# Performance work log

Hardware: AMD Instinct MI355X
Metric: run time of the kernel (lower is better)

Reference implementation:

```python
import jax, jax.numpy as jnp
import numpy as np

N = 16384
E = 524288
IN_DIM, H1, H2 = 256, 128, 64


def setup_inputs() -> dict:
    key = jax.random.key(0)
    ks = jax.random.split(key, 9)
    features = jax.random.normal(ks[0], (N, IN_DIM), dtype=jnp.float32)
    src = jax.random.randint(ks[1], (E,), 0, N, dtype=jnp.int32)
    dst = jax.random.randint(ks[2], (E,), 0, N, dtype=jnp.int32)
    s = 0.1
    W1 = jax.random.normal(ks[3], (IN_DIM, H1), dtype=jnp.float32) * s
    b1 = jnp.zeros((H1,), dtype=jnp.float32)
    W2 = jax.random.normal(ks[4], (H1, H1), dtype=jnp.float32) * s
    b2 = jnp.zeros((H1,), dtype=jnp.float32)
    W3 = jax.random.normal(ks[5], (H1, H2), dtype=jnp.float32) * s
    b3 = jnp.zeros((H2,), dtype=jnp.float32)
    return {"features": features, "src": src, "dst": dst,
            "W1": W1, "b1": b1, "W2": W2, "b2": b2, "W3": W3, "b3": b3}


def _degree_norms(src, dst):
    ones = jnp.ones(src.shape[0], dtype=jnp.float32)
    deg_out = jax.ops.segment_sum(ones, src, num_segments=N)
    deg_in = jax.ops.segment_sum(ones, dst, num_segments=N)
    # allow_zero_in_degree=True with norm='both': clamp degree to min 1
    norm_out = jax.lax.rsqrt(jnp.maximum(deg_out, 1.0))  # [N]
    norm_in = jax.lax.rsqrt(jnp.maximum(deg_in, 1.0))    # [N]
    return norm_out, norm_in


def _graph_conv(h, src, dst, norm_out, norm_in, W, b, relu):
    # DGL GraphConv, norm='both': D_in^{-1/2} A^T (D_out^{-1/2} h) W + b
    h = h * norm_out[:, None]
    msg = h[src]                                   # gather [E, d]
    agg = jax.ops.segment_sum(msg, dst, num_segments=N)  # scatter-add [N, d]
    out = agg * norm_in[:, None] @ W + b
    return jax.nn.relu(out) if relu else out


def reference(features, src, dst, W1, b1, W2, b2, W3, b3):
    norm_out, norm_in = _degree_norms(src, dst)
    h = _graph_conv(features, src, dst, norm_out, norm_in, W1, b1, True)
    h = _graph_conv(h, src, dst, norm_out, norm_in, W2, b2, True)
    z = _graph_conv(h, src, dst, norm_out, norm_in, W3, b3, False)  # [N, H2]
    adj_rec = jax.nn.sigmoid(z @ z.T)  # [N, N]
    return adj_rec, z
```

## Files before the change

### kernel.cpp

```cpp
#include <hip/hip_runtime.h>
#include <hip/hip_bf16.h>

#define NN 16384
#define EE 524288

constexpr int D0 = 256, D1 = 128, D2 = 64;

typedef __attribute__((ext_vector_type(8))) short short8;
typedef __attribute__((ext_vector_type(4))) float f32x4;

__device__ __forceinline__ float b2f(ushort u) {
  union { unsigned int i; float f; } x;
  x.i = ((unsigned int)u) << 16;
  return x.f;
}
__device__ __forceinline__ ushort f2b(float f) {
  __hip_bfloat16 h = __float2bfloat16(f);
  return *reinterpret_cast<ushort*>(&h);
}


__global__ __launch_bounds__(256) void count_deg_kernel(
    const int* __restrict__ src, const int* __restrict__ dst,
    int* __restrict__ deg_out, int* __restrict__ deg_in) {
  int e = blockIdx.x * 256 + threadIdx.x;
  if (e < EE) {
    atomicAdd(&deg_out[src[e]], 1);
    atomicAdd(&deg_in[dst[e]], 1);
  }
}

__global__ __launch_bounds__(256) void scan1_kernel(
    const int* __restrict__ deg_in, int* __restrict__ intra,
    int* __restrict__ part) {
  __shared__ int sc[256];
  int t = threadIdx.x;
  int v = blockIdx.x * 256 + t;
  int d = deg_in[v];
  sc[t] = d;
  __syncthreads();
  for (int off = 1; off < 256; off <<= 1) {
    int add = (t >= off) ? sc[t - off] : 0;
    __syncthreads();
    sc[t] += add;
    __syncthreads();
  }
  intra[v] = sc[t] - d;
  if (t == 255) part[blockIdx.x] = sc[255];
}

__global__ __launch_bounds__(64) void scan2_kernel(
    const int* __restrict__ part, int* __restrict__ partx) {
  __shared__ int p[64];
  int t = threadIdx.x;
  int d = part[t];
  p[t] = d;
  __syncthreads();
  for (int off = 1; off < 64; off <<= 1) {
    int add = (t >= off) ? p[t - off] : 0;
    __syncthreads();
    p[t] += add;
    __syncthreads();
  }
  partx[t] = p[t] - d;
}

__global__ __launch_bounds__(256) void scan3_kernel(
    const int* __restrict__ deg_in, const int* __restrict__ deg_out,
    const int* __restrict__ intra, const int* __restrict__ partx,
    int* __restrict__ row_ptr, int* __restrict__ cursor,
    float* __restrict__ norm_out, float* __restrict__ norm_in) {
  int t = threadIdx.x;
  int v = blockIdx.x * 256 + t;
  int rp = partx[blockIdx.x] + intra[v];
  row_ptr[v] = rp;
  cursor[v] = rp;
  norm_out[v] = rsqrtf(fmaxf((float)deg_out[v], 1.0f));
  norm_in[v]  = rsqrtf(fmaxf((float)deg_in[v], 1.0f));
  if (v == NN - 1) row_ptr[NN] = rp + deg_in[v];
}

__global__ __launch_bounds__(256) void fill_csr_kernel(
    const int* __restrict__ src, const int* __restrict__ dst,
    int* __restrict__ cursor, int* __restrict__ csr_src) {
  int e = blockIdx.x * 256 + threadIdx.x;
  if (e < EE) {
    int pos = atomicAdd(&cursor[dst[e]], 1);
    csr_src[pos] = src[e];
  }
}


template<int DIN, int DOUT, int KC, bool OBF16>
__global__ __launch_bounds__(256) void gemm_kernel(
    const float* __restrict__ h, const float* __restrict__ W,
    const float* __restrict__ norm_out, float* __restrict__ tf,
    ushort* __restrict__ tb) {
  constexpr int W4 = DOUT / 4;
  constexpr int RG = 256 / W4;
  constexpr int RPT = 32 / RG;
  __shared__ float A[32][DIN];
  __shared__ float WC[KC][DOUT];
  int tid = threadIdx.x;
  int r0 = blockIdx.x * 32;
  constexpr int NF4 = 32 * DIN / 4;
  for (int q = tid; q < NF4; q += 256) {
    int r = q / (DIN / 4);
    int c = q % (DIN / 4);
    float4 x = *(const float4*)&h[(size_t)(r0 + r) * DIN + c * 4];
    float no = norm_out[r0 + r];
    x.x *= no; x.y *= no; x.z *= no; x.w *= no;
    *(float4*)&A[r][c * 4] = x;
  }
  int c4 = tid % W4;
  int rg = tid / W4;
  float4 acc[RPT];
#pragma unroll
  for (int j = 0; j < RPT; ++j) acc[j] = make_float4(0.f, 0.f, 0.f, 0.f);

  for (int kc = 0; kc < DIN / KC; ++kc) {
    __syncthreads();
#pragma unroll
    for (int q = 0; q < KC * W4 / 256; ++q)
      ((float4*)WC)[q * 256 + tid] =
          ((const float4*)W)[(size_t)kc * KC * W4 + q * 256 + tid];
    __syncthreads();
#pragma unroll 4
    for (int k2 = 0; k2 < KC; ++k2) {
      float4 w = *(const float4*)&WC[k2][c4 * 4];
#pragma unroll
      for (int j = 0; j < RPT; ++j) {
        float a = A[rg + j * RG][kc * KC + k2];
        acc[j].x += a * w.x; acc[j].y += a * w.y;
        acc[j].z += a * w.z; acc[j].w += a * w.w;
      }
    }
  }
#pragma unroll
  for (int j = 0; j < RPT; ++j) {
    size_t row = (size_t)(r0 + rg + j * RG);
    if (OBF16) {
      ushort4 o;
      o.x = f2b(acc[j].x); o.y = f2b(acc[j].y);
      o.z = f2b(acc[j].z); o.w = f2b(acc[j].w);
      *(ushort4*)&tb[row * DOUT + c4 * 4] = o;
    } else {
      *(float4*)&tf[row * DOUT + c4 * 4] = acc[j];
    }
  }
}


template<int DOUT, bool RELU>
__global__ __launch_bounds__(256) void gather_bf16_kernel(
    const ushort* __restrict__ t, const float* __restrict__ bias,
    const float* __restrict__ norm_in, const int* __restrict__ row_ptr,
    const int* __restrict__ csr, float* __restrict__ out) {
  constexpr int G8 = DOUT / 8;
  constexpr int S = 256 / G8;
  __shared__ float red[S][G8][8];
  int tid = threadIdx.x;
  int c8 = tid % G8, slot = tid / G8;
  int v = blockIdx.x;
  int k0 = row_ptr[v], k1 = row_ptr[v + 1];
  float a[8];
#pragma unroll
  for (int i = 0; i < 8; ++i) a[i] = 0.f;
  for (int k = k0 + slot; k < k1; k += S) {
    int s = csr[k];
    short8 m = *(const short8*)&t[(size_t)s * DOUT + c8 * 8];
#pragma unroll
    for (int i = 0; i < 8; ++i) a[i] += b2f((ushort)m[i]);
  }
#pragma unroll
  for (int i = 0; i < 8; ++i) red[slot][c8][i] = a[i];
  __syncthreads();
#pragma unroll
  for (int s = S / 2; s >= 1; s >>= 1) {
    if (slot < s) {
#pragma unroll
      for (int i = 0; i < 8; ++i) red[slot][c8][i] += red[slot + s][c8][i];
    }
    __syncthreads();
  }
  if (tid < G8) {
    float ni = norm_in[v];
    float o[8];
#pragma unroll
    for (int i = 0; i < 8; ++i) {
      o[i] = red[0][tid][i] * ni + bias[tid * 8 + i];
      if (RELU) o[i] = fmaxf(o[i], 0.f);
    }
    *(float4*)&out[(size_t)v * DOUT + tid * 8] = make_float4(o[0], o[1], o[2], o[3]);
    *(float4*)&out[(size_t)v * DOUT + tid * 8 + 4] = make_float4(o[4], o[5], o[6], o[7]);
  }
}


template<int DOUT, bool RELU>
__global__ __launch_bounds__(256) void gather_f32_kernel(
    const float* __restrict__ t, const float* __restrict__ bias,
    const float* __restrict__ norm_in, const int* __restrict__ row_ptr,
    const int* __restrict__ csr, float* __restrict__ out,
    ushort* __restrict__ zb) {
  constexpr int W4 = DOUT / 4;
  constexpr int S = 256 / W4;
  __shared__ float4 red[256];
  int tid = threadIdx.x;
  int c4 = tid % W4, slot = tid / W4;
  int v = blockIdx.x;
  int k0 = row_ptr[v], k1 = row_ptr[v + 1];
  float4 acc = make_float4(0.f, 0.f, 0.f, 0.f);
  for (int k = k0 + slot; k < k1; k += S) {
    int s = csr[k];
    float4 m = *(const float4*)&t[(size_t)s * DOUT + c4 * 4];
    acc.x += m.x; acc.y += m.y; acc.z += m.z; acc.w += m.w;
  }
  red[tid] = acc;
  __syncthreads();
  if (tid < W4) {
    float4 a = red[tid];
#pragma unroll
    for (int s = 1; s < S; ++s) {
      float4 b = red[s * W4 + tid];
      a.x += b.x; a.y += b.y; a.z += b.z; a.w += b.w;
    }
    float ni = norm_in[v];
    float4 b4 = *(const float4*)&bias[tid * 4];
    a.x = a.x * ni + b4.x; a.y = a.y * ni + b4.y;
    a.z = a.z * ni + b4.z; a.w = a.w * ni + b4.w;
    if (RELU) {
      a.x = fmaxf(a.x, 0.f); a.y = fmaxf(a.y, 0.f);
      a.z = fmaxf(a.z, 0.f); a.w = fmaxf(a.w, 0.f);
    }
    *(float4*)&out[(size_t)v * DOUT + tid * 4] = a;
    ushort4 ob;
    ob.x = f2b(a.x); ob.y = f2b(a.y); ob.z = f2b(a.z); ob.w = f2b(a.w);
    *(ushort4*)&zb[(size_t)v * DOUT + tid * 4] = ob;
  }
}


__global__ __launch_bounds__(256) void adj_mfma_kernel(
    const ushort* __restrict__ zb, float* __restrict__ C) {
  __shared__ ushort SMEM[2 * 128 * 64];
  ushort* ZR = SMEM;
  ushort* ZC = SMEM + 128 * 64;
  int t = threadIdx.x;
  int bx = blockIdx.x & 127, by = blockIdx.x >> 7;
  int row0 = by * 128, col0 = bx * 128;
  {
    int r = t >> 1;
    int ub = (t & 1) * 4;
    const float4* zr = (const float4*)(zb + (size_t)(row0 + r) * 64);
    const float4* zc = (const float4*)(zb + (size_t)(col0 + r) * 64);
    float4* LR = (float4*)ZR;
    float4* LC = (float4*)ZC;
#pragma unroll
    for (int u = 0; u < 4; ++u) {
      int sw = (ub + u) ^ (r & 7);
      LR[r * 8 + sw] = zr[ub + u];
      LC[r * 8 + sw] = zc[ub + u];
    }
  }
  __syncthreads();
  int l = t & 63, w = t >> 6;
  int wy = w >> 1, wx = w & 1;
  int lr = l & 15, lg = l >> 4;
  f32x4 acc[4][4];
#pragma unroll
  for (int i = 0; i < 4; ++i)
#pragma unroll
    for (int j = 0; j < 4; ++j) acc[i][j] = (f32x4){0.f, 0.f, 0.f, 0.f};

#pragma unroll
  for (int ks = 0; ks < 2; ++ks) {
    short8 af[4], bf_[4];
    int u = ks * 4 + lg;
#pragma unroll
    for (int i = 0; i < 4; ++i) {
      int ar = wy * 64 + i * 16 + lr;
      af[i] = *(const short8*)&ZR[ar * 64 + ((u ^ (ar & 7)) << 3)];
      int ac = wx * 64 + i * 16 + lr;
      bf_[i] = *(const short8*)&ZC[ac * 64 + ((u ^ (ac & 7)) << 3)];
    }
#pragma unroll
    for (int i = 0; i < 4; ++i)
#pragma unroll
      for (int j = 0; j < 4; ++j)
        acc[i][j] = __builtin_amdgcn_mfma_f32_16x16x32_bf16(
            bf_[j], af[i], acc[i][j], 0, 0, 0);
  }

  __syncthreads();
  float* scr = ((float*)SMEM) + w * (16 * 68);
  int sr = l >> 4;
  int sc = (l & 15) * 4;
  float* Cbase = C + (size_t)(row0 + wy * 64) * NN + col0 + wx * 64 + sc;
#pragma unroll
  for (int i = 0; i < 4; ++i) {
#pragma unroll
    for (int j = 0; j < 4; ++j) {
      f32x4 o;
      o[0] = __builtin_amdgcn_rcpf(1.0f + __expf(-acc[i][j][0]));
      o[1] = __builtin_amdgcn_rcpf(1.0f + __expf(-acc[i][j][1]));
      o[2] = __builtin_amdgcn_rcpf(1.0f + __expf(-acc[i][j][2]));
      o[3] = __builtin_amdgcn_rcpf(1.0f + __expf(-acc[i][j][3]));
      *(f32x4*)&scr[lr * 68 + j * 16 + lg * 4] = o;
    }
    __syncthreads();
#pragma unroll
    for (int rp = 0; rp < 4; ++rp) {
      int rloc = rp * 4 + sr;
      float4 v = *(const float4*)&scr[rloc * 68 + sc];
      *(float4*)&Cbase[(size_t)(i * 16 + rloc) * NN] = v;
    }
    __syncthreads();
  }
}


extern "C" void kernel_launch(void* const* d_in, const int* in_sizes, int n_in,
                              void* d_out, int out_size, void* d_ws, size_t ws_size,
                              hipStream_t stream) {
  const float* features = (const float*)d_in[0];
  const int* src = (const int*)d_in[1];
  const int* dst = (const int*)d_in[2];
  const float* W1 = (const float*)d_in[3];
  const float* b1 = (const float*)d_in[4];
  const float* W2 = (const float*)d_in[5];
  const float* b2 = (const float*)d_in[6];
  const float* W3 = (const float*)d_in[7];
  const float* b3 = (const float*)d_in[8];

  float* outp = (float*)d_out;
  float* adj = outp;
  float* z = outp + (size_t)NN * NN;

  ushort* tb = (ushort*)adj;
  float* hbuf = adj + (size_t)NN * 64;
  float* t3 = adj + (size_t)NN * 192;

  float* wsf = (float*)d_ws;
  float* norm_out = wsf;
  float* norm_in = wsf + NN;
  int* deg_out = (int*)(wsf + 2 * NN);
  int* deg_in = deg_out + NN;
  int* row_ptr = deg_in + NN;
  int* cursor = row_ptr + NN + 256;
  int* csr_src = cursor + NN;
  ushort* zb = (ushort*)(csr_src + EE);
  int* intra = (int*)(zb + NN * 64);
  int* part = intra + NN;
  int* partx = part + 64;

  hipMemsetAsync(deg_out, 0, 2 * NN * sizeof(int), stream);
  count_deg_kernel<<<EE / 256, 256, 0, stream>>>(src, dst, deg_out, deg_in);
  scan1_kernel<<<64, 256, 0, stream>>>(deg_in, intra, part);
  scan2_kernel<<<1, 64, 0, stream>>>(part, partx);
  scan3_kernel<<<64, 256, 0, stream>>>(deg_in, deg_out, intra, partx,
                                       row_ptr, cursor, norm_out, norm_in);
  fill_csr_kernel<<<EE / 256, 256, 0, stream>>>(src, dst, cursor, csr_src);

  gemm_kernel<D0, D1, 32, true><<<NN / 32, 256, 0, stream>>>(
      features, W1, norm_out, nullptr, tb);
  gather_bf16_kernel<D1, true><<<NN, 256, 0, stream>>>(
      tb, b1, norm_in, row_ptr, csr_src, hbuf);
  gemm_kernel<D1, D1, 64, true><<<NN / 32, 256, 0, stream>>>(
      hbuf, W2, norm_out, nullptr, tb);
  gather_bf16_kernel<D1, true><<<NN, 256, 0, stream>>>(
      tb, b2, norm_in, row_ptr, csr_src, hbuf);
  gemm_kernel<D1, D2, 64, false><<<NN / 32, 256, 0, stream>>>(
      hbuf, W3, norm_out, t3, nullptr);
  gather_f32_kernel<D2, false><<<NN, 256, 0, stream>>>(
      t3, b3, norm_in, row_ptr, csr_src, z, zb);

  adj_mfma_kernel<<<(NN / 128) * (NN / 128), 256, 0, stream>>>(zb, adj);
}
```

Baseline: 392.9 us.

## Fuse degree counting with first-layer GEMM and apply source norm in gather

The layer-1 GEMM (features @ W1) no longer depends on norm_out, so it is merged into the degree-counting kernel: the first 2048 blocks do the atomic degree counts and the remaining blocks compute the unnormalized bf16 GEMM, which removes a launch and runs the GEMM alongside the atomics. The source normalization for layer 1 moves into the first gather, which now reads norm_out per neighbour. This costs an extra scalar load per edge in that gather, and the fused GEMM uses a simple FP32 shared-memory tile of 16 rows per block, which may be slower than the earlier GEMM kernel.

```diff
diff --git a/kernel.cpp b/kernel.cpp
--- a/kernel.cpp
+++ b/kernel.cpp
@@ -20,15 +20,58 @@
 }
 
 
-__global__ __launch_bounds__(256) void count_deg_kernel(
+__global__ __launch_bounds__(256) void count_gemm1_kernel(
     const int* __restrict__ src, const int* __restrict__ dst,
-    int* __restrict__ deg_out, int* __restrict__ deg_in) {
-  int e = blockIdx.x * 256 + threadIdx.x;
-  if (e < EE) {
+    int* __restrict__ deg_out, int* __restrict__ deg_in,
+    const float* __restrict__ features, const float* __restrict__ W1,
+    ushort* __restrict__ t1) {
+  __shared__ float A[16][D0];
+  __shared__ float WC[32][D1];
+  int tid = threadIdx.x;
+  int b = blockIdx.x;
+  if (b < 2048) {
+    int e = b * 256 + tid;
     atomicAdd(&deg_out[src[e]], 1);
     atomicAdd(&deg_in[dst[e]], 1);
-  }
-}
+    return;
+  }
+  int r0 = (b - 2048) * 16;
+  for (int q = tid; q < 16 * D0 / 4; q += 256) {
+    int r = q / (D0 / 4), c = q % (D0 / 4);
+    *(float4*)&A[r][c * 4] =
+        *(const float4*)&features[(size_t)(r0 + r) * D0 + c * 4];
+  }
+  int c4 = tid % 32;
+  int rg = tid / 32;
+  float4 acc[2];
+  acc[0] = make_float4(0.f, 0.f, 0.f, 0.f);
+  acc[1] = make_float4(0.f, 0.f, 0.f, 0.f);
+  for (int kc = 0; kc < D0 / 32; ++kc) {
+    __syncthreads();
+    for (int q = tid; q < 32 * 32; q += 256)
+      ((float4*)WC)[q] = ((const float4*)(W1 + (size_t)kc * 32 * D1))[q];
+    __syncthreads();
+#pragma unroll 4
+    for (int k2 = 0; k2 < 32; ++k2) {
+      float4 w = *(const float4*)&WC[k2][c4 * 4];
+#pragma unroll
+      for (int j = 0; j < 2; ++j) {
+        float a = A[rg + j * 8][kc * 32 + k2];
+        acc[j].x += a * w.x; acc[j].y += a * w.y;
+        acc[j].z += a * w.z; acc[j].w += a * w.w;
+      }
+    }
+  }
+#pragma unroll
+  for (int j = 0; j < 2; ++j) {
+    size_t row = (size_t)(r0 + rg + j * 8);
+    ushort4 o;
+    o.x = f2b(acc[j].x); o.y = f2b(acc[j].y);
+    o.z = f2b(acc[j].z); o.w = f2b(acc[j].w);
+    *(ushort4*)&t1[row * D1 + c4 * 4] = o;
+  }
+}
+
 
 __global__ __launch_bounds__(256) void scan1_kernel(
     const int* __restrict__ deg_in, int* __restrict__ intra,
@@ -151,11 +194,12 @@
 }
 
 
-template<int DOUT, bool RELU>
+template<int DOUT, bool RELU, bool SRCNORM>
 __global__ __launch_bounds__(256) void gather_bf16_kernel(
     const ushort* __restrict__ t, const float* __restrict__ bias,
-    const float* __restrict__ norm_in, const int* __restrict__ row_ptr,
-    const int* __restrict__ csr, float* __restrict__ out) {
+    const float* __restrict__ norm_out, const float* __restrict__ norm_in,
+    const int* __restrict__ row_ptr, const int* __restrict__ csr,
+    float* __restrict__ out) {
   constexpr int G8 = DOUT / 8;
   constexpr int S = 256 / G8;
   __shared__ float red[S][G8][8];
@@ -169,8 +213,14 @@
   for (int k = k0 + slot; k < k1; k += S) {
     int s = csr[k];
     short8 m = *(const short8*)&t[(size_t)s * DOUT + c8 * 8];
-#pragma unroll
-    for (int i = 0; i < 8; ++i) a[i] += b2f((ushort)m[i]);
+    if (SRCNORM) {
+      float no = norm_out[s];
+#pragma unroll
+      for (int i = 0; i < 8; ++i) a[i] += b2f((ushort)m[i]) * no;
+    } else {
+#pragma unroll
+      for (int i = 0; i < 8; ++i) a[i] += b2f((ushort)m[i]);
+    }
   }
 #pragma unroll
   for (int i = 0; i < 8; ++i) red[slot][c8][i] = a[i];
@@ -350,26 +400,25 @@
   int* cursor = row_ptr + NN + 256;
   int* csr_src = cursor + NN;
   ushort* zb = (ushort*)(csr_src + EE);
-  int* intra = (int*)(zb + NN * 64);
+  int* intra = (int*)(zb + (size_t)NN * 64);
   int* part = intra + NN;
   int* partx = part + 64;
 
   hipMemsetAsync(deg_out, 0, 2 * NN * sizeof(int), stream);
-  count_deg_kernel<<<EE / 256, 256, 0, stream>>>(src, dst, deg_out, deg_in);
+  count_gemm1_kernel<<<3072, 256, 0, stream>>>(
+      src, dst, deg_out, deg_in, features, W1, tb);
   scan1_kernel<<<64, 256, 0, stream>>>(deg_in, intra, part);
   scan2_kernel<<<1, 64, 0, stream>>>(part, partx);
   scan3_kernel<<<64, 256, 0, stream>>>(deg_in, deg_out, intra, partx,
                                        row_ptr, cursor, norm_out, norm_in);
   fill_csr_kernel<<<EE / 256, 256, 0, stream>>>(src, dst, cursor, csr_src);
 
-  gemm_kernel<D0, D1, 32, true><<<NN / 32, 256, 0, stream>>>(
-      features, W1, norm_out, nullptr, tb);
-  gather_bf16_kernel<D1, true><<<NN, 256, 0, stream>>>(
-      tb, b1, norm_in, row_ptr, csr_src, hbuf);
+  gather_bf16_kernel<D1, true, true><<<NN, 256, 0, stream>>>(
+      tb, b1, norm_out, norm_in, row_ptr, csr_src, hbuf);
   gemm_kernel<D1, D1, 64, true><<<NN / 32, 256, 0, stream>>>(
       hbuf, W2, norm_out, nullptr, tb);
-  gather_bf16_kernel<D1, true><<<NN, 256, 0, stream>>>(
-      tb, b2, norm_in, row_ptr, csr_src, hbuf);
+  gather_bf16_kernel<D1, true, false><<<NN, 256, 0, stream>>>(
+      tb, b2, norm_out, norm_in, row_ptr, csr_src, hbuf);
   gemm_kernel<D1, D2, 64, false><<<NN / 32, 256, 0, stream>>>(
       hbuf, W3, norm_out, t3, nullptr);
   gather_f32_kernel<D2, false><<<NN, 256, 0, stream>>>(
```

New measurement: 391.4 us. About the same (-0.4%).
